# Optimization experiments

Measured on AMD Instinct MI355X. Metric: run time of the kernel, lower is better.

Reference implementation:

```python
import jax, jax.numpy as jnp
import numpy as np

N_EMBD = 64
N_HEAD = 8
HEAD_SIZE = N_EMBD // N_HEAD  # 8
BLOCK_SIZE = 64
B = 4096
SCALE = N_EMBD ** (-0.5)  # NOTE: source scales by C**-0.5 with C=n_embd, not head_size
EPS = 1e-5


def setup_inputs() -> dict:
    key = jax.random.key(0)
    ks = jax.random.split(key, 12)
    s = 0.02
    return {
        "x": jax.random.normal(ks[0], (B, BLOCK_SIZE, N_EMBD), jnp.float32),
        # per-head q/k/v projections packed as [C, H, hs] (no bias in source)
        "Wq": jax.random.normal(ks[1], (N_EMBD, N_HEAD, HEAD_SIZE), jnp.float32) * s,
        "Wk": jax.random.normal(ks[2], (N_EMBD, N_HEAD, HEAD_SIZE), jnp.float32) * s,
        "Wv": jax.random.normal(ks[3], (N_EMBD, N_HEAD, HEAD_SIZE), jnp.float32) * s,
        "Wo": jax.random.normal(ks[4], (N_EMBD, N_EMBD), jnp.float32) * s,
        "bo": jnp.zeros((N_EMBD,), jnp.float32),
        "W1": jax.random.normal(ks[5], (N_EMBD, 4 * N_EMBD), jnp.float32) * s,
        "b1": jnp.zeros((4 * N_EMBD,), jnp.float32),
        "W2": jax.random.normal(ks[6], (4 * N_EMBD, N_EMBD), jnp.float32) * s,
        "b2": jnp.zeros((N_EMBD,), jnp.float32),
        "g1": jnp.ones((N_EMBD,), jnp.float32),
        "be1": jnp.zeros((N_EMBD,), jnp.float32),
        "g2": jnp.ones((N_EMBD,), jnp.float32),
        "be2": jnp.zeros((N_EMBD,), jnp.float32),
    }


def _layernorm(x, g, b):
    mu = jnp.mean(x, axis=-1, keepdims=True)
    var = jnp.mean(jnp.square(x - mu), axis=-1, keepdims=True)
    return (x - mu) * jax.lax.rsqrt(var + EPS) * g + b


def reference(x, Wq, Wk, Wv, Wo, bo, W1, b1, W2, b2, g1, be1, g2, be2):
    Bb, T, C = x.shape
    # --- multi-head causal self-attention (dropout = identity in eval) ---
    h = _layernorm(x, g1, be1)
    q = jnp.einsum('btc,chd->bhtd', h, Wq)
    k = jnp.einsum('btc,chd->bhtd', h, Wk)
    v = jnp.einsum('btc,chd->bhtd', h, Wv)
    wei = jnp.einsum('bhtd,bhsd->bhts', q, k) * SCALE
    mask = jnp.tril(jnp.ones((T, T), dtype=bool))
    wei = jnp.where(mask, wei, -jnp.inf)
    wei = jax.nn.softmax(wei, axis=-1)
    attn = jnp.einsum('bhts,bhsd->bhtd', wei, v)
    attn = attn.transpose(0, 2, 1, 3).reshape(Bb, T, C)  # concat heads
    x = x + attn @ Wo + bo
    # --- feed-forward ---
    h2 = _layernorm(x, g2, be2)
    ff = jax.nn.relu(h2 @ W1 + b1) @ W2 + b2
    return x + ff
```

## Files before the change

### kernel.cpp

```cpp
#include <hip/hip_runtime.h>
#include <hip/hip_bf16.h>


typedef __attribute__((ext_vector_type(8))) short short8;
typedef __attribute__((ext_vector_type(4))) float f32x4;

#if __has_builtin(__builtin_amdgcn_exp2f)
#define EXP2F(x) __builtin_amdgcn_exp2f(x)
#else
#define EXP2F(x) __expf((x) * 0.69314718056f)
#endif
#if __has_builtin(__builtin_amdgcn_rcpf)
#define RCPF(x) __builtin_amdgcn_rcpf(x)
#else
#define RCPF(x) (1.0f / (x))
#endif

#define ST  72
#define STU 136
#define OH  0
#define OKK 4608
#define OV  9216
#define OP  13896
#define OU  4608
#define NSH 18504

__device__ __forceinline__ short f2bf(float f) {
    unsigned int u = __float_as_uint(f);
    u += 0x7fffu + ((u >> 16) & 1u);
    return (short)(u >> 16);
}
__device__ __forceinline__ unsigned pk2(float a, float b) {
    float2 t; t.x = a; t.y = b;
    __hip_bfloat162 h = __float22bfloat162_rn(t);
    unsigned u; __builtin_memcpy(&u, &h, 4); return u;
}
__device__ __forceinline__ f32x4 mfma16(short8 a, short8 b, f32x4 c) {
    return __builtin_amdgcn_mfma_f32_16x16x32_bf16(a, b, c, 0, 0, 0);
}

__global__ __launch_bounds__(64) void prepack_kernel(
    const float* __restrict__ Wq, const float* __restrict__ Wk,
    const float* __restrict__ Wv, const float* __restrict__ Wo,
    const float* __restrict__ W1, const float* __restrict__ W2,
    short* __restrict__ ws)
{
    int gid = blockIdx.x * 64 + threadIdx.x;
    int lane = gid & 63;
    int fid  = gid >> 6;
    int quad = lane >> 4, nn = lane & 15;
    short8 o;
    if (fid < 24) {
        int tile = fid >> 1, ks = fid & 1;
        const float* Ws = (tile < 4) ? Wq : ((tile < 8) ? Wk : Wv);
        float scale = (tile < 4) ? 0.18033688011f : 1.0f;
        int col = (tile & 3) * 16 + nn;
#pragma unroll
        for (int j = 0; j < 8; ++j)
            o[j] = f2bf(Ws[(ks * 32 + quad * 8 + j) * 64 + col] * scale);
    } else if (fid < 32) {
        int idx = fid - 24, nt = idx >> 1, ks = idx & 1;
#pragma unroll
        for (int j = 0; j < 8; ++j)
            o[j] = f2bf(Wo[(ks * 32 + quad * 8 + j) * 64 + nt * 16 + nn]);
    } else if (fid < 64) {
        int idx = fid - 32, c = idx >> 3, tile = (idx >> 1) & 3, ks = idx & 1;
#pragma unroll
        for (int j = 0; j < 8; ++j)
            o[j] = f2bf(W1[(ks * 32 + quad * 8 + j) * 256 + c * 64 + tile * 16 + nn]);
    } else {
        int idx = fid - 64, c = idx >> 3, nt = (idx >> 1) & 3, ks = idx & 1;
#pragma unroll
        for (int j = 0; j < 8; ++j)
            o[j] = f2bf(W2[(c * 64 + ks * 32 + quad * 8 + j) * 64 + nt * 16 + nn]);
    }
    *(short8*)(ws + (size_t)gid * 8) = o;
}

__global__ __launch_bounds__(256, 4) void block_kernel(
    const float* __restrict__ x,
    const float* __restrict__ bo,
    const float* __restrict__ b1,
    const float* __restrict__ b2,
    const float* __restrict__ g1, const float* __restrict__ be1,
    const float* __restrict__ g2, const float* __restrict__ be2,
    const short8* __restrict__ WB,
    float* __restrict__ out)
{
    __shared__ short sm[NSH];
    const int tid  = threadIdx.x;
    const int wv   = tid >> 6;
    const int lane = tid & 63;
    const int quad = lane >> 4;
    const int nn   = lane & 15;
    const int t_my = wv * 16 + nn;
    const int b    = blockIdx.x;
    const float* xb = x + (size_t)b * 4096;
    const f32x4 zf = {0.f, 0.f, 0.f, 0.f};
    const short8 z8 = {0, 0, 0, 0, 0, 0, 0, 0};

    if (tid < ST) sm[OV + 64 * ST + tid] = (short)0x3F80;
    float xr[16];
    float gv[4], bv[4];
#pragma unroll
    for (int nt = 0; nt < 4; ++nt) { gv[nt] = g1[nt * 16 + nn]; bv[nt] = be1[nt * 16 + nn]; }
#pragma unroll
    for (int nt = 0; nt < 4; ++nt)
#pragma unroll
        for (int r = 0; r < 4; ++r)
            xr[nt * 4 + r] = xb[(wv * 16 + quad * 4 + r) * 64 + nt * 16 + nn];
#pragma unroll
    for (int r = 0; r < 4; ++r) {
        float s1 = 0.f, s2 = 0.f;
#pragma unroll
        for (int nt = 0; nt < 4; ++nt) { float v = xr[nt * 4 + r]; s1 += v; s2 += v * v; }
        s1 += __shfl_xor(s1, 1); s1 += __shfl_xor(s1, 2); s1 += __shfl_xor(s1, 4); s1 += __shfl_xor(s1, 8);
        s2 += __shfl_xor(s2, 1); s2 += __shfl_xor(s2, 2); s2 += __shfl_xor(s2, 4); s2 += __shfl_xor(s2, 8);
        float mu = s1 * 0.015625f;
        float rstd = rsqrtf(s2 * 0.015625f - mu * mu + 1e-5f);
        int base = OH + (wv * 16 + quad * 4 + r) * ST + nn;
        float h0 = (xr[0 + r]  - mu) * rstd * gv[0] + bv[0];
        float h1 = (xr[4 + r]  - mu) * rstd * gv[1] + bv[1];
        float h2 = (xr[8 + r]  - mu) * rstd * gv[2] + bv[2];
        float h3 = (xr[12 + r] - mu) * rstd * gv[3] + bv[3];
        unsigned pA = pk2(h0, h1), pB = pk2(h2, h3);
        sm[base +  0] = (short)pA;
        sm[base + 16] = (short)(pA >> 16);
        sm[base + 32] = (short)pB;
        sm[base + 48] = (short)(pB >> 16);
    }

    unsigned qp[8];
    {
        short8 hf0 = *(const short8*)&sm[OH + t_my * ST + quad * 8];
        short8 hf1 = *(const short8*)&sm[OH + t_my * ST + 32 + quad * 8];
#pragma unroll
        for (int jt = 0; jt < 4; ++jt) {
            f32x4 a = mfma16(WB[(size_t)(jt * 2 + 0) * 64 + lane], hf0, zf);
            a = mfma16(WB[(size_t)(jt * 2 + 1) * 64 + lane], hf1, a);
            qp[jt * 2 + 0] = pk2(a[0], a[1]);
            qp[jt * 2 + 1] = pk2(a[2], a[3]);
        }
#pragma unroll
        for (int jt = 0; jt < 4; ++jt) {
            f32x4 a = mfma16(WB[(size_t)((4 + jt) * 2 + 0) * 64 + lane], hf0, zf);
            a = mfma16(WB[(size_t)((4 + jt) * 2 + 1) * 64 + lane], hf1, a);
            uint2 w; w.x = pk2(a[0], a[1]); w.y = pk2(a[2], a[3]);
            *(uint2*)&sm[OKK + t_my * ST + jt * 16 + quad * 4] = w;
        }
#pragma unroll
        for (int dt = 0; dt < 4; ++dt) {
            f32x4 a = mfma16(hf0, WB[(size_t)((8 + dt) * 2 + 0) * 64 + lane], zf);
            a = mfma16(hf1, WB[(size_t)((8 + dt) * 2 + 1) * 64 + lane], a);
            uint2 w; w.x = pk2(a[0], a[1]); w.y = pk2(a[2], a[3]);
            *(uint2*)&sm[OV + (dt * 16 + nn) * ST + wv * 16 + quad * 4] = w;
        }
    }
    __syncthreads();

    const bool keep0 = (quad * 4 + 0) <= nn, keep1 = (quad * 4 + 1) <= nn;
    const bool keep2 = (quad * 4 + 2) <= nn, keep3 = (quad * 4 + 3) <= nn;
    const int arow_base = (nn < 8) ? nn : 64;
    const int arow_step = (nn < 8) ? 8 : 0;
    const int nks = (wv < 2) ? 1 : 2;
    const int zhi = nks * 2;
    for (int mt = wv + 1; mt < zhi; ++mt) {
        uint2 w; w.x = 0u; w.y = 0u;
        *(uint2*)&sm[OP + t_my * ST + mt * 16 + quad * 4] = w;
    }
#pragma unroll 2
    for (int h = 0; h < 8; ++h) {
        short8 bq;
        {
            int qsA = ((h & 1) * 2) * 16 + nn, qsB = qsA + 16;
            int qi = (h >> 1) * 2;
            union { unsigned u[4]; short8 s; } bb;
            bb.u[0] = __shfl(qp[qi + 0], qsA);
            bb.u[1] = __shfl(qp[qi + 1], qsA);
            bb.u[2] = __shfl(qp[qi + 0], qsB);
            bb.u[3] = __shfl(qp[qi + 1], qsB);
            bq = bb.s;
        }
#pragma unroll
        for (int mt = 0; mt < 4; ++mt) {
            if (mt <= wv) {
                short8 ak = z8;
                if (quad == 0) ak = *(const short8*)&sm[OKK + (mt * 16 + nn) * ST + h * 8];
                f32x4 s = mfma16(ak, bq, zf);
                float e0 = EXP2F(s[0]), e1 = EXP2F(s[1]), e2 = EXP2F(s[2]), e3 = EXP2F(s[3]);
                if (mt == wv) {
                    e0 = keep0 ? e0 : 0.f; e1 = keep1 ? e1 : 0.f;
                    e2 = keep2 ? e2 : 0.f; e3 = keep3 ? e3 : 0.f;
                }
                uint2 w; w.x = pk2(e0, e1); w.y = pk2(e2, e3);
                *(uint2*)&sm[OP + t_my * ST + mt * 16 + quad * 4] = w;
            }
        }
        const int arow = arow_base + h * arow_step;
        f32x4 pv = zf;
#pragma unroll
        for (int ks = 0; ks < 2; ++ks) {
            if (ks < nks) {
                short8 av = *(const short8*)&sm[OV + arow * ST + ks * 32 + quad * 8];
                short8 bp = *(const short8*)&sm[OP + t_my * ST + ks * 32 + quad * 8];
                pv = mfma16(av, bp, pv);
            }
        }
        float denom = __shfl(pv[0], 32 + nn);
        float rd = RCPF(denom);
        if (quad < 2) {
            uint2 w; w.x = pk2(pv[0] * rd, pv[1] * rd); w.y = pk2(pv[2] * rd, pv[3] * rd);
            *(uint2*)&sm[OH + t_my * ST + h * 8 + quad * 4] = w;
        }
    }

    {
        short8 aa0 = *(const short8*)&sm[OH + t_my * ST + quad * 8];
        short8 aa1 = *(const short8*)&sm[OH + t_my * ST + 32 + quad * 8];
#pragma unroll
        for (int nt = 0; nt < 4; ++nt) {
            f32x4 oa = mfma16(aa0, WB[(size_t)(24 + nt * 2 + 0) * 64 + lane], zf);
            oa = mfma16(aa1, WB[(size_t)(24 + nt * 2 + 1) * 64 + lane], oa);
            float bov = bo[nt * 16 + nn];
#pragma unroll
            for (int r = 0; r < 4; ++r) xr[nt * 4 + r] += oa[r] + bov;
        }
    }
#pragma unroll
    for (int nt = 0; nt < 4; ++nt) { gv[nt] = g2[nt * 16 + nn]; bv[nt] = be2[nt * 16 + nn]; }
#pragma unroll
    for (int r = 0; r < 4; ++r) {
        float s1 = 0.f, s2 = 0.f;
#pragma unroll
        for (int nt = 0; nt < 4; ++nt) { float v = xr[nt * 4 + r]; s1 += v; s2 += v * v; }
        s1 += __shfl_xor(s1, 1); s1 += __shfl_xor(s1, 2); s1 += __shfl_xor(s1, 4); s1 += __shfl_xor(s1, 8);
        s2 += __shfl_xor(s2, 1); s2 += __shfl_xor(s2, 2); s2 += __shfl_xor(s2, 4); s2 += __shfl_xor(s2, 8);
        float mu = s1 * 0.015625f;
        float rstd = rsqrtf(s2 * 0.015625f - mu * mu + 1e-5f);
        int base = OP + (wv * 16 + quad * 4 + r) * ST + nn;
        float h0 = (xr[0 + r]  - mu) * rstd * gv[0] + bv[0];
        float h1 = (xr[4 + r]  - mu) * rstd * gv[1] + bv[1];
        float h2 = (xr[8 + r]  - mu) * rstd * gv[2] + bv[2];
        float h3 = (xr[12 + r] - mu) * rstd * gv[3] + bv[3];
        unsigned pA = pk2(h0, h1), pB = pk2(h2, h3);
        sm[base +  0] = (short)pA;
        sm[base + 16] = (short)(pA >> 16);
        sm[base + 32] = (short)pB;
        sm[base + 48] = (short)(pB >> 16);
    }
    short8 h2f0 = *(const short8*)&sm[OP + t_my * ST + quad * 8];
    short8 h2f1 = *(const short8*)&sm[OP + t_my * ST + 32 + quad * 8];
    __syncthreads();

    f32x4 fa[4];
#pragma unroll
    for (int nt = 0; nt < 4; ++nt) fa[nt] = zf;
#pragma unroll
    for (int c = 0; c < 2; ++c) {
#pragma unroll
        for (int tile = 0; tile < 8; ++tile) {
            int gc = c * 8 + tile;
            int fid = 32 + (gc >> 2) * 8 + (gc & 3) * 2;
            f32x4 u = mfma16(WB[(size_t)fid * 64 + lane], h2f0, zf);
            u = mfma16(WB[(size_t)(fid + 1) * 64 + lane], h2f1, u);
            const float4 bb = *(const float4*)&b1[gc * 16 + quad * 4];
            float u0 = fmaxf(u[0] + bb.x, 0.f), u1 = fmaxf(u[1] + bb.y, 0.f);
            float u2 = fmaxf(u[2] + bb.z, 0.f), u3 = fmaxf(u[3] + bb.w, 0.f);
            uint2 w; w.x = pk2(u0, u1); w.y = pk2(u2, u3);
            *(uint2*)&sm[OU + t_my * STU + tile * 16 + quad * 4] = w;
        }
#pragma unroll
        for (int ks = 0; ks < 4; ++ks) {
            short8 au = *(const short8*)&sm[OU + t_my * STU + ks * 32 + quad * 8];
            int gk = c * 4 + ks;
            int fidb = 64 + (gk >> 1) * 8 + (gk & 1);
#pragma unroll
            for (int nt = 0; nt < 4; ++nt)
                fa[nt] = mfma16(au, WB[(size_t)(fidb + nt * 2) * 64 + lane], fa[nt]);
        }
    }

    float* ob = out + (size_t)b * 4096;
#pragma unroll
    for (int nt = 0; nt < 4; ++nt) {
        float b2v = b2[nt * 16 + nn];
#pragma unroll
        for (int r = 0; r < 4; ++r)
            ob[(wv * 16 + quad * 4 + r) * 64 + nt * 16 + nn] = xr[nt * 4 + r] + fa[nt][r] + b2v;
    }
}

extern "C" void kernel_launch(void* const* d_in, const int* in_sizes, int n_in,
                              void* d_out, int out_size, void* d_ws, size_t ws_size,
                              hipStream_t stream) {
    const float* x   = (const float*)d_in[0];
    const float* Wq  = (const float*)d_in[1];
    const float* Wk  = (const float*)d_in[2];
    const float* Wv  = (const float*)d_in[3];
    const float* Wo  = (const float*)d_in[4];
    const float* bo  = (const float*)d_in[5];
    const float* W1  = (const float*)d_in[6];
    const float* b1  = (const float*)d_in[7];
    const float* W2  = (const float*)d_in[8];
    const float* b2  = (const float*)d_in[9];
    const float* g1  = (const float*)d_in[10];
    const float* be1 = (const float*)d_in[11];
    const float* g2  = (const float*)d_in[12];
    const float* be2 = (const float*)d_in[13];
    short* ws = (short*)d_ws;
    prepack_kernel<<<dim3(96), dim3(64), 0, stream>>>(Wq, Wk, Wv, Wo, W1, W2, ws);
    const int nb = in_sizes[0] / 4096;
    block_kernel<<<dim3(nb), dim3(256), 0, stream>>>(
        x, bo, b1, b2, g1, be1, g2, be2, (const short8*)ws, (float*)d_out);
}
```

Measured before the change: 201.2 us.

## Partition K/V and FFN weight tiles across waves to cut redundant weight loads

The K/V projection and the FFN now give each wave a fixed slice of weight columns across all 64 rows, instead of every wave loading every weight fragment for its own 16 rows. Each wave reads its weight fragments once and reuses them over four row tiles, which reduces global/L2 traffic for WB per wave. In return the kernel needs extra __syncthreads barriers, shares the hidden activations across waves through LDS, and adds an LDS staging pass to reassemble the FFN output before the residual add and store.

```diff
diff --git a/kernel.cpp b/kernel.cpp
--- a/kernel.cpp
+++ b/kernel.cpp
@@ -129,9 +129,14 @@
         sm[base + 32] = (short)pB;
         sm[base + 48] = (short)(pB >> 16);
     }
+    __syncthreads();
 
     unsigned qp[8];
     {
+        const short8 wk0 = WB[(size_t)((4 + wv) * 2 + 0) * 64 + lane];
+        const short8 wk1 = WB[(size_t)((4 + wv) * 2 + 1) * 64 + lane];
+        const short8 wv0 = WB[(size_t)((8 + wv) * 2 + 0) * 64 + lane];
+        const short8 wv1 = WB[(size_t)((8 + wv) * 2 + 1) * 64 + lane];
         short8 hf0 = *(const short8*)&sm[OH + t_my * ST + quad * 8];
         short8 hf1 = *(const short8*)&sm[OH + t_my * ST + 32 + quad * 8];
 #pragma unroll
@@ -142,18 +147,15 @@
             qp[jt * 2 + 1] = pk2(a[2], a[3]);
         }
 #pragma unroll
-        for (int jt = 0; jt < 4; ++jt) {
-            f32x4 a = mfma16(WB[(size_t)((4 + jt) * 2 + 0) * 64 + lane], hf0, zf);
-            a = mfma16(WB[(size_t)((4 + jt) * 2 + 1) * 64 + lane], hf1, a);
-            uint2 w; w.x = pk2(a[0], a[1]); w.y = pk2(a[2], a[3]);
-            *(uint2*)&sm[OKK + t_my * ST + jt * 16 + quad * 4] = w;
-        }
-#pragma unroll
-        for (int dt = 0; dt < 4; ++dt) {
-            f32x4 a = mfma16(hf0, WB[(size_t)((8 + dt) * 2 + 0) * 64 + lane], zf);
-            a = mfma16(hf1, WB[(size_t)((8 + dt) * 2 + 1) * 64 + lane], a);
-            uint2 w; w.x = pk2(a[0], a[1]); w.y = pk2(a[2], a[3]);
-            *(uint2*)&sm[OV + (dt * 16 + nn) * ST + wv * 16 + quad * 4] = w;
+        for (int rt = 0; rt < 4; ++rt) {
+            short8 hA = *(const short8*)&sm[OH + (rt * 16 + nn) * ST + quad * 8];
+            short8 hB = *(const short8*)&sm[OH + (rt * 16 + nn) * ST + 32 + quad * 8];
+            f32x4 ka = mfma16(wk0, hA, zf); ka = mfma16(wk1, hB, ka);
+            uint2 w1; w1.x = pk2(ka[0], ka[1]); w1.y = pk2(ka[2], ka[3]);
+            *(uint2*)&sm[OKK + (rt * 16 + nn) * ST + wv * 16 + quad * 4] = w1;
+            f32x4 va = mfma16(hA, wv0, zf); va = mfma16(hB, wv1, va);
+            uint2 w2; w2.x = pk2(va[0], va[1]); w2.y = pk2(va[2], va[3]);
+            *(uint2*)&sm[OV + (wv * 16 + nn) * ST + rt * 16 + quad * 4] = w2;
         }
     }
     __syncthreads();
@@ -248,45 +250,72 @@
         sm[base + 32] = (short)pB;
         sm[base + 48] = (short)(pB >> 16);
     }
-    short8 h2f0 = *(const short8*)&sm[OP + t_my * ST + quad * 8];
-    short8 h2f1 = *(const short8*)&sm[OP + t_my * ST + 32 + quad * 8];
     __syncthreads();
 
+    short8 h2r[4][2];
+#pragma unroll
+    for (int rt = 0; rt < 4; ++rt) {
+        h2r[rt][0] = *(const short8*)&sm[OP + (rt * 16 + nn) * ST + quad * 8];
+        h2r[rt][1] = *(const short8*)&sm[OP + (rt * 16 + nn) * ST + 32 + quad * 8];
+    }
     f32x4 fa[4];
 #pragma unroll
-    for (int nt = 0; nt < 4; ++nt) fa[nt] = zf;
+    for (int rt = 0; rt < 4; ++rt) fa[rt] = zf;
 #pragma unroll
     for (int c = 0; c < 2; ++c) {
 #pragma unroll
-        for (int tile = 0; tile < 8; ++tile) {
-            int gc = c * 8 + tile;
+        for (int g = 0; g < 2; ++g) {
+            int gc = c * 8 + wv * 2 + g;
             int fid = 32 + (gc >> 2) * 8 + (gc & 3) * 2;
-            f32x4 u = mfma16(WB[(size_t)fid * 64 + lane], h2f0, zf);
-            u = mfma16(WB[(size_t)(fid + 1) * 64 + lane], h2f1, u);
+            short8 wf0 = WB[(size_t)fid * 64 + lane];
+            short8 wf1 = WB[(size_t)(fid + 1) * 64 + lane];
             const float4 bb = *(const float4*)&b1[gc * 16 + quad * 4];
-            float u0 = fmaxf(u[0] + bb.x, 0.f), u1 = fmaxf(u[1] + bb.y, 0.f);
-            float u2 = fmaxf(u[2] + bb.z, 0.f), u3 = fmaxf(u[3] + bb.w, 0.f);
-            uint2 w; w.x = pk2(u0, u1); w.y = pk2(u2, u3);
-            *(uint2*)&sm[OU + t_my * STU + tile * 16 + quad * 4] = w;
-        }
-#pragma unroll
-        for (int ks = 0; ks < 4; ++ks) {
-            short8 au = *(const short8*)&sm[OU + t_my * STU + ks * 32 + quad * 8];
-            int gk = c * 4 + ks;
-            int fidb = 64 + (gk >> 1) * 8 + (gk & 1);
-#pragma unroll
-            for (int nt = 0; nt < 4; ++nt)
-                fa[nt] = mfma16(au, WB[(size_t)(fidb + nt * 2) * 64 + lane], fa[nt]);
-        }
-    }
+#pragma unroll
+            for (int rt = 0; rt < 4; ++rt) {
+                f32x4 u = mfma16(wf0, h2r[rt][0], zf);
+                u = mfma16(wf1, h2r[rt][1], u);
+                float u0 = fmaxf(u[0] + bb.x, 0.f), u1 = fmaxf(u[1] + bb.y, 0.f);
+                float u2 = fmaxf(u[2] + bb.z, 0.f), u3 = fmaxf(u[3] + bb.w, 0.f);
+                uint2 w; w.x = pk2(u0, u1); w.y = pk2(u2, u3);
+                *(uint2*)&sm[OU + (rt * 16 + nn) * STU + (wv * 2 + g) * 16 + quad * 4] = w;
+            }
+        }
+        __syncthreads();
+#pragma unroll
+        for (int kl = 0; kl < 4; ++kl) {
+            int fidb = 64 + (c * 2 + (kl >> 1)) * 8 + wv * 2 + (kl & 1);
+            short8 w2f = WB[(size_t)fidb * 64 + lane];
+#pragma unroll
+            for (int rt = 0; rt < 4; ++rt) {
+                short8 au = *(const short8*)&sm[OU + (rt * 16 + nn) * STU + kl * 32 + quad * 8];
+                fa[rt] = mfma16(au, w2f, fa[rt]);
+            }
+        }
+        if (c == 0) __syncthreads();
+    }
+    {
+        float* yr = (wv < 2) ? (float*)sm : (float*)(sm + OP);
+        const int ycol = (wv & 1) * 16 + nn;
+#pragma unroll
+        for (int rt = 0; rt < 4; ++rt)
+#pragma unroll
+            for (int r = 0; r < 4; ++r)
+                yr[(rt * 16 + quad * 4 + r) * 34 + ycol] = fa[rt][r];
+    }
+    __syncthreads();
 
     float* ob = out + (size_t)b * 4096;
+    const float* yA = (const float*)sm;
+    const float* yB = (const float*)(sm + OP);
 #pragma unroll
     for (int nt = 0; nt < 4; ++nt) {
+        const float* ys = (nt < 2) ? yA : yB;
         float b2v = b2[nt * 16 + nn];
 #pragma unroll
-        for (int r = 0; r < 4; ++r)
-            ob[(wv * 16 + quad * 4 + r) * 64 + nt * 16 + nn] = xr[nt * 4 + r] + fa[nt][r] + b2v;
+        for (int r = 0; r < 4; ++r) {
+            float yv = ys[(wv * 16 + quad * 4 + r) * 34 + (nt & 1) * 16 + nn];
+            ob[(wv * 16 + quad * 4 + r) * 64 + nt * 16 + nn] = xr[nt * 4 + r] + yv + b2v;
+        }
     }
 }
 
```

Result: faster. 196.9 us (-2.1%).
